# Performance work log

Measured on AMD Instinct MI355X. Metric: run time of the kernel, lower is better.

Reference implementation:

```python
import jax, jax.numpy as jnp
import numpy as np

STRIDE = 1
PAD = 3  # kernel_size // 2 = 7 // 2


def setup_inputs() -> dict:
    key = jax.random.key(0)
    k1, k2, k3 = jax.random.split(key, 3)
    B, Cin, T = 32, 128, 4096
    K, Cout, ks = 4, 256, 7
    x = jax.random.normal(k1, (B, Cin, T), dtype=jnp.float32)
    weight = jax.random.normal(k2, (K, Cout, Cin, ks), dtype=jnp.float32) * 0.01
    bias = jnp.zeros((K, Cout), dtype=jnp.float32)
    rw = jax.random.normal(k3, (K, Cin), dtype=jnp.float32) * 0.05
    rb = jnp.zeros((K,), dtype=jnp.float32)
    return {"x": x, "weight": weight, "bias": bias, "rw": rw, "rb": rb}


def reference(x, weight, bias, rw, rb):
    # x: [B, Cin, T]; weight: [K, Cout, Cin, ks]; bias: [K, Cout]
    K, Cout, Cin, ks = weight.shape
    B = x.shape[0]
    # routing: adaptive avg pool over T -> Linear -> softmax
    pooled = jnp.mean(x, axis=-1)                      # [B, Cin]
    alpha = jax.nn.softmax(pooled @ rw.T + rb, axis=-1)  # [B, K]
    # all K conv branches in one conv by folding K into out-channels
    w_all = weight.reshape(K * Cout, Cin, ks)
    y = jax.lax.conv_general_dilated(
        x, w_all, window_strides=(STRIDE,), padding=[(PAD, PAD)],
        dimension_numbers=("NCH", "OIH", "NCH"))      # [B, K*Cout, T']
    Tp = y.shape[-1]
    y = y.reshape(B, K, Cout, Tp) + bias[None, :, :, None]
    # softmax-routed weighted sum over the K branches
    out = jnp.einsum("bk,bkct->bct", alpha, y)         # [B, Cout, T']
    return out
```

## Files before the change

kernel.cpp:

```cpp
#include <hip/hip_runtime.h>
#include <stdint.h>


#define TP 4102

#define XT_OFF     0u
#define WT_OFF     33603584u
#define WEFF_OFF   37273600u
#define POOLED_OFF 51953664u
#define ALPHA_OFF  51970048u
#define BIAS_OFF   51970560u

typedef short short8 __attribute__((ext_vector_type(8)));
typedef float f32x4 __attribute__((ext_vector_type(4)));

__device__ __forceinline__ unsigned short f2bf(float f) {
  unsigned int u = __builtin_bit_cast(unsigned int, f);
  u += 0x7fffu + ((u >> 16) & 1u);
  return (unsigned short)(u >> 16);
}

__global__ __launch_bounds__(256) void k_transpose_pool(
    const float* __restrict__ x, unsigned short* __restrict__ xt,
    float* __restrict__ pooled) {
  __shared__ __align__(16) unsigned short xs[128 * 136];
  __shared__ float pbuf[128 * 33];
  int blk = blockIdx.x;
  int b = blk >> 5, tc = blk & 31;
  int t0 = tc << 7;
  int tid = threadIdx.x;
  int lane32 = tid & 31, grp8 = tid >> 5;

  #pragma unroll
  for (int i = 0; i < 16; ++i) {
    int ci = i * 8 + grp8;
    const float4 v = *(const float4*)(x + (size_t)(b * 128 + ci) * 4096 + t0 + lane32 * 4);
    unsigned short h0 = f2bf(v.x), h1 = f2bf(v.y), h2 = f2bf(v.z), h3 = f2bf(v.w);
    uint2 pk;
    pk.x = (unsigned)h0 | ((unsigned)h1 << 16);
    pk.y = (unsigned)h2 | ((unsigned)h3 << 16);
    *(uint2*)(&xs[ci * 136 + lane32 * 4]) = pk;
    pbuf[ci * 33 + lane32] = v.x + v.y + v.z + v.w;
  }
  __syncthreads();
  if (tid < 128) {
    float s = 0.f;
    #pragma unroll
    for (int l = 0; l < 32; ++l) s += pbuf[tid * 33 + l];
    atomicAdd(&pooled[b * 128 + tid], s);
  }
  #pragma unroll
  for (int it = 0; it < 8; ++it) {
    int idx = it * 256 + tid;
    int tr = idx & 127, g = idx >> 7;
    unsigned short h[8];
    #pragma unroll
    for (int u = 0; u < 8; ++u) h[u] = xs[(g * 8 + u) * 136 + tr];
    uint4 o;
    o.x = (unsigned)h[0] | ((unsigned)h[1] << 16);
    o.y = (unsigned)h[2] | ((unsigned)h[3] << 16);
    o.z = (unsigned)h[4] | ((unsigned)h[5] << 16);
    o.w = (unsigned)h[6] | ((unsigned)h[7] << 16);
    *(uint4*)(xt + ((size_t)(b * 16 + g) * TP + 3 + t0 + tr) * 8) = o;
  }
  uint4 z; z.x = z.y = z.z = z.w = 0;
  if (tc == 0 && tid < 64) {
    int g = tid >> 2, pr = tid & 3;
    if (pr < 3) *(uint4*)(xt + ((size_t)(b * 16 + g) * TP + pr) * 8) = z;
  }
  if (tc == 31 && tid < 64) {
    int g = tid >> 2, pr = tid & 3;
    if (pr < 3) *(uint4*)(xt + ((size_t)(b * 16 + g) * TP + 4099 + pr) * 8) = z;
  }
}

__global__ __launch_bounds__(256) void k_wt(const float* __restrict__ w,
                                            float* __restrict__ wt) {
  int gid = blockIdx.x * 256 + threadIdx.x;
  int ci = gid & 127;
  int kc = gid >> 7;
  const float* src = w + (size_t)gid * 7;
  #pragma unroll
  for (int s = 0; s < 7; ++s)
    wt[((size_t)kc * 7 + s) * 128 + ci] = src[s];
}

__global__ __launch_bounds__(128) void k_alpha(
    const float* __restrict__ pooled, const float* __restrict__ rw,
    const float* __restrict__ rb, const float* __restrict__ bias,
    float* __restrict__ alpha, float* __restrict__ bias_eff) {
  __shared__ float red[4][128];
  __shared__ float al[4];
  int b = blockIdx.x, tid = threadIdx.x;
  float p = pooled[b * 128 + tid] * (1.0f / 4096.0f);
  #pragma unroll
  for (int k = 0; k < 4; ++k) red[k][tid] = p * rw[k * 128 + tid];
  __syncthreads();
  if (tid < 4) {
    float s = rb[tid];
    for (int j = 0; j < 128; ++j) s += red[tid][j];
    red[tid][0] = s;
  }
  __syncthreads();
  if (tid == 0) {
    float m = red[0][0];
    for (int k = 1; k < 4; ++k) m = fmaxf(m, red[k][0]);
    float e0 = __expf(red[0][0] - m), e1 = __expf(red[1][0] - m);
    float e2 = __expf(red[2][0] - m), e3 = __expf(red[3][0] - m);
    float inv = 1.0f / (e0 + e1 + e2 + e3);
    al[0] = e0 * inv; al[1] = e1 * inv; al[2] = e2 * inv; al[3] = e3 * inv;
    #pragma unroll
    for (int k = 0; k < 4; ++k) alpha[b * 4 + k] = al[k];
  }
  __syncthreads();
  #pragma unroll
  for (int cc = 0; cc < 2; ++cc) {
    int c = cc * 128 + tid;
    float s = 0.f;
    #pragma unroll
    for (int k = 0; k < 4; ++k) s += al[k] * bias[k * 256 + c];
    bias_eff[b * 256 + c] = s;
  }
}

__global__ __launch_bounds__(256) void k_fold(const float* __restrict__ wt,
                                              const float* __restrict__ alpha,
                                              unsigned short* __restrict__ weff) {
  int idx = blockIdx.x * 256 + threadIdx.x;
  int g = idx & 7;
  int c = (idx >> 3) & 127;
  int rest = idx >> 10;
  int chunk = rest % 14;
  int bcb = rest / 14;
  int cb = bcb & 1, b = bcb >> 1;
  int s = chunk >> 1, half = chunk & 1;
  int cout = cb * 128 + c;
  int gs = g ^ (c & 7);
  float a[4];
  #pragma unroll
  for (int k = 0; k < 4; ++k) a[k] = alpha[b * 4 + k];
  float acc8[8];
  #pragma unroll
  for (int j = 0; j < 8; ++j) acc8[j] = 0.f;
  #pragma unroll
  for (int k = 0; k < 4; ++k) {
    const float* src = wt + (((size_t)(k * 256 + cout) * 7 + s) * 128 + half * 64 + g * 8);
    #pragma unroll
    for (int j = 0; j < 8; ++j) acc8[j] += a[k] * src[j];
  }
  unsigned short h[8];
  #pragma unroll
  for (int j = 0; j < 8; ++j) h[j] = f2bf(acc8[j]);
  uint4 o;
  o.x = (unsigned)h[0] | ((unsigned)h[1] << 16);
  o.y = (unsigned)h[2] | ((unsigned)h[3] << 16);
  o.z = (unsigned)h[4] | ((unsigned)h[5] << 16);
  o.w = (unsigned)h[6] | ((unsigned)h[7] << 16);
  *(uint4*)(weff + (size_t)(bcb * 14 + chunk) * 8192 + (size_t)c * 64 + gs * 8) = o;
}

__global__ __launch_bounds__(256) void k_conv(
    const unsigned short* __restrict__ xt, const unsigned short* __restrict__ weff,
    const float* __restrict__ bias_eff, float* __restrict__ out) {
  __shared__ __align__(16) unsigned short xs[134 * 136];
  __shared__ __align__(16) unsigned short wsb[2][8192];
  int blk = blockIdx.x;
  int b = blk >> 6, cb = (blk >> 5) & 1, tb = blk & 31;
  int bcb = b * 2 + cb;
  int tid = threadIdx.x;
  int wave = tid >> 6, lane = tid & 63;
  int q = lane >> 4, n16 = lane & 15;
  int wm = wave & 1, wn = wave >> 1;
  int t00 = tb << 7;

  #pragma unroll 1
  for (int g = 0; g < 16; ++g) {
    if (tid < 134) {
      uint4 v = *(const uint4*)(xt + ((size_t)(b * 16 + g) * TP + t00 + tid) * 8);
      *(uint4*)(&xs[tid * 136 + g * 8]) = v;
    }
  }
  const uint4* wsrc = (const uint4*)(weff + (size_t)bcb * 14 * 8192);
  uint4 wv[4];
  #pragma unroll
  for (int it = 0; it < 4; ++it) wv[it] = wsrc[it * 256 + tid];
  #pragma unroll
  for (int it = 0; it < 4; ++it) ((uint4*)wsb[0])[it * 256 + tid] = wv[it];
  __syncthreads();

  f32x4 acc[4][4];
  #pragma unroll
  for (int mi = 0; mi < 4; ++mi)
    #pragma unroll
    for (int ni = 0; ni < 4; ++ni)
      acc[mi][ni] = (f32x4){0.f, 0.f, 0.f, 0.f};

  for (int chunk = 0; chunk < 14; ++chunk) {
    if (chunk + 1 < 14) {
      const uint4* srcN = wsrc + (size_t)(chunk + 1) * 1024;
      #pragma unroll
      for (int it = 0; it < 4; ++it) wv[it] = srcN[it * 256 + tid];
    }
    int cur = chunk & 1;
    int s = chunk >> 1, half = chunk & 1;
    const unsigned short* wb = wsb[cur];
    #pragma unroll
    for (int kk = 0; kk < 2; ++kk) {
      short8 av[4], bv[4];
      #pragma unroll
      for (int mi = 0; mi < 4; ++mi) {
        int c = wm * 64 + mi * 16 + n16;
        int gl = (kk * 4 + q) ^ (c & 7);
        av[mi] = *(const short8*)(&wb[c * 64 + gl * 8]);
      }
      #pragma unroll
      for (int ni = 0; ni < 4; ++ni) {
        int tt = wn * 64 + ni * 16 + n16;
        bv[ni] = *(const short8*)(&xs[(tt + s) * 136 + half * 64 + kk * 32 + q * 8]);
      }
      #pragma unroll
      for (int mi = 0; mi < 4; ++mi)
        #pragma unroll
        for (int ni = 0; ni < 4; ++ni)
          acc[mi][ni] = __builtin_amdgcn_mfma_f32_16x16x32_bf16(
              av[mi], bv[ni], acc[mi][ni], 0, 0, 0);
    }
    if (chunk + 1 < 14) {
      #pragma unroll
      for (int it = 0; it < 4; ++it) ((uint4*)wsb[cur ^ 1])[it * 256 + tid] = wv[it];
    }
    __syncthreads();
  }

  int crow0 = b * 256 + cb * 128;
  #pragma unroll
  for (int mi = 0; mi < 4; ++mi) {
    #pragma unroll
    for (int r = 0; r < 4; ++r) {
      int c = wm * 64 + mi * 16 + q * 4 + r;
      float bb = bias_eff[crow0 + c];
      float* orow = out + (size_t)(crow0 + c) * 4096 + t00;
      #pragma unroll
      for (int ni = 0; ni < 4; ++ni)
        orow[wn * 64 + ni * 16 + n16] = acc[mi][ni][r] + bb;
    }
  }
}

extern "C" void kernel_launch(void* const* d_in, const int* in_sizes, int n_in,
                              void* d_out, int out_size, void* d_ws, size_t ws_size,
                              hipStream_t stream) {
  const float* x    = (const float*)d_in[0];
  const float* w    = (const float*)d_in[1];
  const float* bias = (const float*)d_in[2];
  const float* rw   = (const float*)d_in[3];
  const float* rb   = (const float*)d_in[4];
  float* out = (float*)d_out;
  char* ws = (char*)d_ws;
  unsigned short* xt   = (unsigned short*)(ws + XT_OFF);
  float* wt            = (float*)(ws + WT_OFF);
  unsigned short* weff = (unsigned short*)(ws + WEFF_OFF);
  float* pooled        = (float*)(ws + POOLED_OFF);
  float* alpha         = (float*)(ws + ALPHA_OFF);
  float* bias_eff      = (float*)(ws + BIAS_OFF);

  hipMemsetAsync(pooled, 0, 32 * 128 * sizeof(float), stream);
  hipLaunchKernelGGL(k_transpose_pool, dim3(1024), dim3(256), 0, stream, x, xt, pooled);
  hipLaunchKernelGGL(k_wt,    dim3(512),  dim3(256), 0, stream, w, wt);
  hipLaunchKernelGGL(k_alpha, dim3(32),   dim3(128), 0, stream, pooled, rw, rb, bias, alpha, bias_eff);
  hipLaunchKernelGGL(k_fold,  dim3(3584), dim3(256), 0, stream, wt, alpha, weff);
  hipLaunchKernelGGL(k_conv,  dim3(2048), dim3(256), 0, stream, xt, weff, bias_eff, out);
}
```

Measured before the change: 284.2 us.

## Pre-swizzle folded weights into MFMA fragment order and load directly from global

The fold kernel now reads the original weight layout directly, which removes the separate weight-transpose kernel, and writes the bf16 effective weights already arranged in per-lane MFMA A-fragment order. The conv kernel drops the double-buffered LDS weight staging and per-chunk barriers. It instead prefetches A fragments from global (L2) into registers one step ahead. It also changes the x tile LDS layout to group-major and raises occupancy via launch bounds of 4 blocks. This trades LDS traffic and barriers for more global/L2 reads of the weights by every block, plus register pressure from the prefetch.

```diff
diff --git a/kernel.cpp b/kernel.cpp
--- a/kernel.cpp
+++ b/kernel.cpp
@@ -5,11 +5,10 @@
 #define TP 4102
 
 #define XT_OFF     0u
-#define WT_OFF     33603584u
-#define WEFF_OFF   37273600u
-#define POOLED_OFF 51953664u
-#define ALPHA_OFF  51970048u
-#define BIAS_OFF   51970560u
+#define WEFF_OFF   33603584u
+#define POOLED_OFF 48283648u
+#define ALPHA_OFF  48300032u
+#define BIAS_OFF   48300544u
 
 typedef short short8 __attribute__((ext_vector_type(8)));
 typedef float f32x4 __attribute__((ext_vector_type(4)));
@@ -74,17 +73,6 @@
   }
 }
 
-__global__ __launch_bounds__(256) void k_wt(const float* __restrict__ w,
-                                            float* __restrict__ wt) {
-  int gid = blockIdx.x * 256 + threadIdx.x;
-  int ci = gid & 127;
-  int kc = gid >> 7;
-  const float* src = w + (size_t)gid * 7;
-  #pragma unroll
-  for (int s = 0; s < 7; ++s)
-    wt[((size_t)kc * 7 + s) * 128 + ci] = src[s];
-}
-
 __global__ __launch_bounds__(128) void k_alpha(
     const float* __restrict__ pooled, const float* __restrict__ rw,
     const float* __restrict__ rb, const float* __restrict__ bias,
@@ -123,19 +111,21 @@
   }
 }
 
-__global__ __launch_bounds__(256) void k_fold(const float* __restrict__ wt,
+__global__ __launch_bounds__(256) void k_fold(const float* __restrict__ w,
                                               const float* __restrict__ alpha,
                                               unsigned short* __restrict__ weff) {
   int idx = blockIdx.x * 256 + threadIdx.x;
-  int g = idx & 7;
-  int c = (idx >> 3) & 127;
+  int n16 = idx & 15;
+  int q = (idx >> 4) & 3;
+  int cblk = (idx >> 6) & 7;
+  int kk = (idx >> 9) & 1;
   int rest = idx >> 10;
   int chunk = rest % 14;
   int bcb = rest / 14;
   int cb = bcb & 1, b = bcb >> 1;
   int s = chunk >> 1, half = chunk & 1;
-  int cout = cb * 128 + c;
-  int gs = g ^ (c & 7);
+  int cout = cb * 128 + cblk * 16 + n16;
+  int ci0 = half * 64 + (kk * 4 + q) * 8;
   float a[4];
   #pragma unroll
   for (int k = 0; k < 4; ++k) a[k] = alpha[b * 4 + k];
@@ -144,9 +134,9 @@
   for (int j = 0; j < 8; ++j) acc8[j] = 0.f;
   #pragma unroll
   for (int k = 0; k < 4; ++k) {
-    const float* src = wt + (((size_t)(k * 256 + cout) * 7 + s) * 128 + half * 64 + g * 8);
-    #pragma unroll
-    for (int j = 0; j < 8; ++j) acc8[j] += a[k] * src[j];
+    const float* src = w + ((size_t)(k * 256 + cout) * 128 + ci0) * 7 + s;
+    #pragma unroll
+    for (int j = 0; j < 8; ++j) acc8[j] += a[k] * src[j * 7];
   }
   unsigned short h[8];
   #pragma unroll
@@ -156,14 +146,13 @@
   o.y = (unsigned)h[2] | ((unsigned)h[3] << 16);
   o.z = (unsigned)h[4] | ((unsigned)h[5] << 16);
   o.w = (unsigned)h[6] | ((unsigned)h[7] << 16);
-  *(uint4*)(weff + (size_t)(bcb * 14 + chunk) * 8192 + (size_t)c * 64 + gs * 8) = o;
-}
-
-__global__ __launch_bounds__(256) void k_conv(
+  *(uint4*)(weff + (size_t)idx * 8) = o;
+}
+
+__global__ __launch_bounds__(256, 4) void k_conv(
     const unsigned short* __restrict__ xt, const unsigned short* __restrict__ weff,
     const float* __restrict__ bias_eff, float* __restrict__ out) {
-  __shared__ __align__(16) unsigned short xs[134 * 136];
-  __shared__ __align__(16) unsigned short wsb[2][8192];
+  __shared__ __align__(16) unsigned short xs[16 * 136 * 8];
   int blk = blockIdx.x;
   int b = blk >> 6, cb = (blk >> 5) & 1, tb = blk & 31;
   int bcb = b * 2 + cb;
@@ -173,19 +162,22 @@
   int wm = wave & 1, wn = wave >> 1;
   int t00 = tb << 7;
 
-  #pragma unroll 1
-  for (int g = 0; g < 16; ++g) {
-    if (tid < 134) {
-      uint4 v = *(const uint4*)(xt + ((size_t)(b * 16 + g) * TP + t00 + tid) * 8);
-      *(uint4*)(&xs[tid * 136 + g * 8]) = v;
-    }
-  }
-  const uint4* wsrc = (const uint4*)(weff + (size_t)bcb * 14 * 8192);
-  uint4 wv[4];
-  #pragma unroll
-  for (int it = 0; it < 4; ++it) wv[it] = wsrc[it * 256 + tid];
-  #pragma unroll
-  for (int it = 0; it < 4; ++it) ((uint4*)wsb[0])[it * 256 + tid] = wv[it];
+  const unsigned short* xtb = xt + (size_t)b * 16 * TP * 8;
+  #pragma unroll
+  for (int it = 0; it < 8; ++it) {
+    int idx = it * 256 + tid;
+    int g = idx >> 7, row = idx & 127;
+    uint4 v = *(const uint4*)(xtb + ((size_t)g * TP + t00 + row) * 8);
+    *(uint4*)(&xs[(g * 136 + row) * 8]) = v;
+  }
+  if (tid < 128) {
+    int g = tid >> 3, r8 = tid & 7;
+    if (r8 < 6) {
+      int row = 128 + r8;
+      uint4 v = *(const uint4*)(xtb + ((size_t)g * TP + t00 + row) * 8);
+      *(uint4*)(&xs[(g * 136 + row) * 8]) = v;
+    }
+  }
   __syncthreads();
 
   f32x4 acc[4][4];
@@ -195,41 +187,35 @@
     for (int ni = 0; ni < 4; ++ni)
       acc[mi][ni] = (f32x4){0.f, 0.f, 0.f, 0.f};
 
-  for (int chunk = 0; chunk < 14; ++chunk) {
-    if (chunk + 1 < 14) {
-      const uint4* srcN = wsrc + (size_t)(chunk + 1) * 1024;
-      #pragma unroll
-      for (int it = 0; it < 4; ++it) wv[it] = srcN[it * 256 + tid];
-    }
-    int cur = chunk & 1;
-    int s = chunk >> 1, half = chunk & 1;
-    const unsigned short* wb = wsb[cur];
-    #pragma unroll
-    for (int kk = 0; kk < 2; ++kk) {
-      short8 av[4], bv[4];
-      #pragma unroll
-      for (int mi = 0; mi < 4; ++mi) {
-        int c = wm * 64 + mi * 16 + n16;
-        int gl = (kk * 4 + q) ^ (c & 7);
-        av[mi] = *(const short8*)(&wb[c * 64 + gl * 8]);
-      }
-      #pragma unroll
-      for (int ni = 0; ni < 4; ++ni) {
-        int tt = wn * 64 + ni * 16 + n16;
-        bv[ni] = *(const short8*)(&xs[(tt + s) * 136 + half * 64 + kk * 32 + q * 8]);
-      }
+  const short8* wfrag = (const short8*)weff + (size_t)bcb * 14336 + (wm * 4) * 64 + lane;
+
+  short8 av[4];
+  #pragma unroll
+  for (int mi = 0; mi < 4; ++mi) av[mi] = wfrag[mi * 64];
+
+  #pragma unroll 2
+  for (int step = 0; step < 28; ++step) {
+    int s = step >> 2, half = (step >> 1) & 1, kk = step & 1;
+    short8 avn[4];
+    if (step < 27) {
       #pragma unroll
       for (int mi = 0; mi < 4; ++mi)
-        #pragma unroll
-        for (int ni = 0; ni < 4; ++ni)
-          acc[mi][ni] = __builtin_amdgcn_mfma_f32_16x16x32_bf16(
-              av[mi], bv[ni], acc[mi][ni], 0, 0, 0);
-    }
-    if (chunk + 1 < 14) {
+        avn[mi] = wfrag[(step + 1) * 512 + mi * 64];
+    }
+    short8 bv[4];
+    #pragma unroll
+    for (int ni = 0; ni < 4; ++ni) {
+      int tt = wn * 64 + ni * 16 + n16;
+      bv[ni] = *(const short8*)(&xs[((half * 8 + kk * 4 + q) * 136 + tt + s) * 8]);
+    }
+    #pragma unroll
+    for (int mi = 0; mi < 4; ++mi)
       #pragma unroll
-      for (int it = 0; it < 4; ++it) ((uint4*)wsb[cur ^ 1])[it * 256 + tid] = wv[it];
-    }
-    __syncthreads();
+      for (int ni = 0; ni < 4; ++ni)
+        acc[mi][ni] = __builtin_amdgcn_mfma_f32_16x16x32_bf16(
+            av[mi], bv[ni], acc[mi][ni], 0, 0, 0);
+    #pragma unroll
+    for (int mi = 0; mi < 4; ++mi) av[mi] = avn[mi];
   }
 
   int crow0 = b * 256 + cb * 128;
@@ -258,7 +244,6 @@
   float* out = (float*)d_out;
   char* ws = (char*)d_ws;
   unsigned short* xt   = (unsigned short*)(ws + XT_OFF);
-  float* wt            = (float*)(ws + WT_OFF);
   unsigned short* weff = (unsigned short*)(ws + WEFF_OFF);
   float* pooled        = (float*)(ws + POOLED_OFF);
   float* alpha         = (float*)(ws + ALPHA_OFF);
@@ -266,8 +251,7 @@
 
   hipMemsetAsync(pooled, 0, 32 * 128 * sizeof(float), stream);
   hipLaunchKernelGGL(k_transpose_pool, dim3(1024), dim3(256), 0, stream, x, xt, pooled);
-  hipLaunchKernelGGL(k_wt,    dim3(512),  dim3(256), 0, stream, w, wt);
   hipLaunchKernelGGL(k_alpha, dim3(32),   dim3(128), 0, stream, pooled, rw, rb, bias, alpha, bias_eff);
-  hipLaunchKernelGGL(k_fold,  dim3(3584), dim3(256), 0, stream, wt, alpha, weff);
+  hipLaunchKernelGGL(k_fold,  dim3(3584), dim3(256), 0, stream, w, alpha, weff);
   hipLaunchKernelGGL(k_conv,  dim3(2048), dim3(256), 0, stream, xt, weff, bias_eff, out);
 }
```

New measurement: 299.4 us. 5.3% more time.
